# Performance work log

Hardware: AMD Instinct MI355X
Metric: run time of the kernel (lower is better)

## Reference

```python
import jax, jax.numpy as jnp
import numpy as np

B, N, DIM, H = 4, 2048, 1024, 8
HD = DIM // H
SCALE = HD ** -0.5


def setup_inputs() -> dict:
    key = jax.random.key(0)
    ks = jax.random.split(key, 9)
    inp = {
        "q": jax.random.normal(ks[0], (B, N, DIM), dtype=jnp.float32),
        "k": jax.random.normal(ks[1], (B, N, DIM), dtype=jnp.float32),
        "v": jax.random.normal(ks[2], (B, N, DIM), dtype=jnp.float32),
        "trans_mat": jax.random.normal(ks[3], (B, N, N), dtype=jnp.float32),
        # torch Linear weights: [out_features, in_features]; qkv_bias=False
        "Wq": jax.random.normal(ks[4], (DIM, DIM), dtype=jnp.float32) * (DIM ** -0.5),
        "Wk": jax.random.normal(ks[5], (DIM, DIM), dtype=jnp.float32) * (DIM ** -0.5),
        "Wv": jax.random.normal(ks[6], (DIM, DIM), dtype=jnp.float32) * (DIM ** -0.5),
        "Wp": jax.random.normal(ks[7], (DIM, DIM), dtype=jnp.float32) * (DIM ** -0.5),
        "bp": jax.random.normal(ks[8], (DIM,), dtype=jnp.float32) * 0.01,
    }
    return inp


def reference(q, k, v, trans_mat, Wq, Wk, Wv, Wp, bp):
    Bq, Nq, C = q.shape
    # project and split heads: [B, H, N, HD]
    qh = (q @ Wq.T).reshape(Bq, Nq, H, HD).transpose(0, 2, 1, 3)
    kh = (k @ Wk.T).reshape(Bq, -1, H, HD).transpose(0, 2, 1, 3)
    vh = (v @ Wv.T).reshape(Bq, -1, H, HD).transpose(0, 2, 1, 3)
    # scaled scores gated elementwise by trans_mat (broadcast over heads)
    scores = jnp.einsum("bhqd,bhkd->bhqk", qh, kh) * SCALE
    gated = scores * trans_mat[:, None, :, :]
    # softmax over full row, then zero out positions where gated == 0
    sm = jax.nn.softmax(gated, axis=-1)
    attn = jnp.where(gated != 0, sm, jnp.zeros((), dtype=sm.dtype))
    x = jnp.einsum("bhqk,bhkd->bhqd", attn, vh)
    x = x.transpose(0, 2, 1, 3).reshape(Bq, Nq, C)
    return x @ Wp.T + bp
```

## Files before the change

### kernel.cpp

```cpp
#include <hip/hip_runtime.h>
#include <hip/hip_bf16.h>
#include <stdint.h>

#define B_    4
#define N_    2048
#define DIM_  1024
#define H_    8
#define HD_   128
#define MTOK  (B_ * N_)
#define SCALE_  0.08838834764831845f
#define LOG2E_  1.4426950408889634f
#define QSCALE_ (SCALE_ * LOG2E_)

typedef unsigned short u16;
typedef __attribute__((ext_vector_type(4))) float f32x4;
typedef __attribute__((ext_vector_type(8))) short s16x8;
typedef __attribute__((ext_vector_type(8))) u16  u16x8;
typedef __attribute__((ext_vector_type(4))) u16  u16x4;

__device__ __forceinline__ u16 f2bf(float f) {
    uint32_t i = __builtin_bit_cast(uint32_t, f);
    return (u16)((i + 0x7FFFu + ((i >> 16) & 1u)) >> 16);
}

__device__ __forceinline__ void gl_lds16(const u16* g, u16* l) {
    __builtin_amdgcn_global_load_lds((const __attribute__((address_space(1))) void*)g,
                                     (__attribute__((address_space(3))) void*)l,
                                     16, 0, 0);
}

__global__ __launch_bounds__(256) void cvt_f32_bf16(const float* __restrict__ src,
                                                    u16* __restrict__ dst, int n) {
    int i = (blockIdx.x * 256 + threadIdx.x) * 4;
    int stride = gridDim.x * 256 * 4;
    for (; i < n; i += stride) {
        float4 v = *(const float4*)(src + i);
        u16x4 o;
        o.x = f2bf(v.x); o.y = f2bf(v.y); o.z = f2bf(v.z); o.w = f2bf(v.w);
        *(u16x4*)(dst + i) = o;
    }
}

template <int MODE>
__global__ __launch_bounds__(256) void gemm_bt(const u16* __restrict__ A,
                                               const u16* __restrict__ Bt,
                                               void* __restrict__ Cout,
                                               const float* __restrict__ bias,
                                               float scale, int M, int NN, int K) {
    __shared__ __align__(16) u16 lga[128 * 64];
    __shared__ __align__(16) u16 lgb[128 * 64];
    const int tid  = threadIdx.x;
    const int lane = tid & 63, wave = tid >> 6;
    const int wm = wave >> 1, wn = wave & 1;
    const int row0 = blockIdx.y * 128, col0 = blockIdx.x * 128;

    f32x4 acc[4][4] = {};

    auto stageLds = [&](const u16* G, u16* L, int rowbase, int k0) {
        #pragma unroll
        for (int i = 0; i < 4; i++) {
            int rb = wave * 32 + i * 8;
            int r  = rb + (lane >> 3);
            int cc = (lane & 7) ^ (lane >> 3);
            gl_lds16(G + (size_t)(rowbase + r) * K + k0 + cc * 8, L + rb * 64);
        }
    };

    for (int k0 = 0; k0 < K; k0 += 64) {
        stageLds(A,  lga, row0, k0);
        stageLds(Bt, lgb, col0, k0);
        __syncthreads();
        #pragma unroll
        for (int kk = 0; kk < 2; kk++) {
            s16x8 af[4], bfr[4];
            #pragma unroll
            for (int mi = 0; mi < 4; mi++) {
                int r = wm * 64 + mi * 16 + (lane & 15);
                int sc = (kk * 4 + (lane >> 4)) ^ (lane & 7);
                af[mi] = *(const s16x8*)(&lga[r * 64 + sc * 8]);
            }
            #pragma unroll
            for (int ni = 0; ni < 4; ni++) {
                int r = wn * 64 + ni * 16 + (lane & 15);
                int sc = (kk * 4 + (lane >> 4)) ^ (lane & 7);
                bfr[ni] = *(const s16x8*)(&lgb[r * 64 + sc * 8]);
            }
            #pragma unroll
            for (int mi = 0; mi < 4; mi++)
                #pragma unroll
                for (int ni = 0; ni < 4; ni++)
                    acc[mi][ni] = __builtin_amdgcn_mfma_f32_16x16x32_bf16(
                        af[mi], bfr[ni], acc[mi][ni], 0, 0, 0);
        }
        __syncthreads();
    }

    #pragma unroll
    for (int mi = 0; mi < 4; mi++) {
        #pragma unroll
        for (int ni = 0; ni < 4; ni++) {
            #pragma unroll
            for (int r = 0; r < 4; r++) {
                int grow = row0 + wm * 64 + mi * 16 + ((lane >> 4) << 2) + r;
                int gcol = col0 + wn * 64 + ni * 16 + (lane & 15);
                float vv = acc[mi][ni][r];
                if (MODE == 2) {
                    ((float*)Cout)[(size_t)grow * NN + gcol] = vv + bias[gcol];
                } else {
                    vv *= scale;
                    int bb = grow >> 11, n = grow & (N_ - 1);
                    int hh = gcol >> 7,  d = gcol & (HD_ - 1);
                    size_t idx = (MODE == 0)
                        ? ((size_t)(bb * H_ + hh) * N_ + n) * HD_ + d
                        : ((size_t)(bb * H_ + hh) * HD_ + d) * N_ + n;
                    ((u16*)Cout)[idx] = f2bf(vv);
                }
            }
        }
    }
}

__global__ __launch_bounds__(512) void attn_kernel(const u16* __restrict__ Qh,
                                                   const u16* __restrict__ Kh,
                                                   const u16* __restrict__ Vt,
                                                   const float* __restrict__ trans,
                                                   u16* __restrict__ xout) {
    __shared__ __align__(16) u16 kt[64 * 128];
    __shared__ __align__(16) u16 vt[128 * 64];
    __shared__ __align__(16) u16 plds[8][16 * 72];

    const int tid = threadIdx.x, lane = tid & 63, wave = tid >> 6;
    const int qt = blockIdx.x, h = blockIdx.y, b = blockIdx.z;
    const int qrow_base = qt * 128 + wave * 16;

    const u16* Qbh = Qh + (size_t)(b * H_ + h) * N_ * HD_;
    const u16* Kbh = Kh + (size_t)(b * H_ + h) * N_ * HD_;
    const u16* Vbh = Vt + (size_t)(b * H_ + h) * HD_ * N_;
    const float* trow = trans + (size_t)b * N_ * N_
                      + (size_t)(qrow_base + ((lane >> 4) << 2)) * N_ + (lane & 15);

    s16x8 qf[4];
    {
        int r = qrow_base + (lane & 15);
        #pragma unroll
        for (int kd = 0; kd < 4; kd++)
            qf[kd] = *(const s16x8*)(Qbh + (size_t)r * HD_ + kd * 32 + ((lane >> 4) << 3));
    }

    auto stageKV = [&](int kv0) {
        int rbk = wave * 8, rbv = wave * 16;
        #pragma unroll
        for (int j = 0; j < 2; j++) {
            int c = j * 64 + lane;
            int rk = rbk + (c >> 4);
            int ck = (c & 15) ^ (rk & 15);
            gl_lds16(Kbh + (size_t)(kv0 + rk) * HD_ + ck * 8, kt + rbk * 128 + j * 512);
            int rv = rbv + (c >> 3);
            int cv = (c & 7) ^ (rv & 7);
            gl_lds16(Vbh + (size_t)rv * N_ + kv0 + cv * 8, vt + rbv * 64 + j * 512);
        }
    };

    float m[4], l[4];
    #pragma unroll
    for (int r = 0; r < 4; r++) { m[r] = -3.0e38f; l[r] = 0.f; }
    f32x4 ao[8] = {};

    for (int kv0 = 0; kv0 < N_; kv0 += 64) {
        stageKV(kv0);
        __syncthreads();

        f32x4 s[4] = {};
        #pragma unroll
        for (int kd = 0; kd < 4; kd++)
            #pragma unroll
            for (int ni = 0; ni < 4; ni++) {
                int r = ni * 16 + (lane & 15);
                int sc = (kd * 4 + (lane >> 4)) ^ (lane & 15);
                s16x8 bfr = *(const s16x8*)(&kt[r * 128 + sc * 8]);
                s[ni] = __builtin_amdgcn_mfma_f32_16x16x32_bf16(qf[kd], bfr, s[ni], 0, 0, 0);
            }

        float pmax[4] = {-3.0e38f, -3.0e38f, -3.0e38f, -3.0e38f};
        #pragma unroll
        for (int ni = 0; ni < 4; ni++)
            #pragma unroll
            for (int r = 0; r < 4; r++) {
                float tt = trow[(size_t)r * N_ + kv0 + ni * 16];
                float gg = s[ni][r] * tt;
                s[ni][r] = gg;
                pmax[r] = fmaxf(pmax[r], gg);
            }
        #pragma unroll
        for (int r = 0; r < 4; r++) {
            float p = pmax[r];
            p = fmaxf(p, __shfl_xor(p, 1));
            p = fmaxf(p, __shfl_xor(p, 2));
            p = fmaxf(p, __shfl_xor(p, 4));
            p = fmaxf(p, __shfl_xor(p, 8));
            pmax[r] = p;
        }
        bool need = false;
        #pragma unroll
        for (int r = 0; r < 4; r++) need = need || (pmax[r] > m[r] + 8.0f);
        if (__any(need)) {
            #pragma unroll
            for (int r = 0; r < 4; r++) {
                float mn = fmaxf(m[r], pmax[r]);
                float sfv = __builtin_amdgcn_exp2f(m[r] - mn);
                m[r] = mn;
                l[r] *= sfv;
                #pragma unroll
                for (int t = 0; t < 8; t++) ao[t][r] *= sfv;
            }
        }
        float rowsum[4] = {0.f, 0.f, 0.f, 0.f};
        u16* pw = &plds[wave][0];
        #pragma unroll
        for (int ni = 0; ni < 4; ni++)
            #pragma unroll
            for (int r = 0; r < 4; r++) {
                float gg = s[ni][r];
                float e = __builtin_amdgcn_exp2f(gg - m[r]);
                rowsum[r] += e;
                float pe = (gg != 0.0f) ? e : 0.0f;
                pw[(((lane >> 4) << 2) + r) * 72 + ni * 16 + (lane & 15)] = f2bf(pe);
            }
        #pragma unroll
        for (int r = 0; r < 4; r++) {
            float ssum = rowsum[r];
            ssum += __shfl_xor(ssum, 1);
            ssum += __shfl_xor(ssum, 2);
            ssum += __shfl_xor(ssum, 4);
            ssum += __shfl_xor(ssum, 8);
            l[r] += ssum;
        }
        #pragma unroll
        for (int kk = 0; kk < 2; kk++) {
            s16x8 pa = *(const s16x8*)(&pw[(lane & 15) * 72 + kk * 32 + ((lane >> 4) << 3)]);
            #pragma unroll
            for (int t = 0; t < 8; t++) {
                int r = t * 16 + (lane & 15);
                int sc = (kk * 4 + (lane >> 4)) ^ (lane & 7);
                s16x8 vb = *(const s16x8*)(&vt[r * 64 + sc * 8]);
                ao[t] = __builtin_amdgcn_mfma_f32_16x16x32_bf16(pa, vb, ao[t], 0, 0, 0);
            }
        }
        __syncthreads();
    }

    #pragma unroll
    for (int r = 0; r < 4; r++) {
        float inv = 1.0f / l[r];
        int n = qrow_base + ((lane >> 4) << 2) + r;
        u16* orow = xout + ((size_t)(b * N_ + n)) * DIM_ + h * HD_;
        #pragma unroll
        for (int t = 0; t < 8; t++)
            orow[t * 16 + (lane & 15)] = f2bf(ao[t][r] * inv);
    }
}

extern "C" void kernel_launch(void* const* d_in, const int* in_sizes, int n_in,
                              void* d_out, int out_size, void* d_ws, size_t ws_size,
                              hipStream_t stream) {
    const float* q     = (const float*)d_in[0];
    const float* k     = (const float*)d_in[1];
    const float* v     = (const float*)d_in[2];
    const float* trans = (const float*)d_in[3];
    const float* Wq    = (const float*)d_in[4];
    const float* Wk    = (const float*)d_in[5];
    const float* Wv    = (const float*)d_in[6];
    const float* Wp    = (const float*)d_in[7];
    const float* bp    = (const float*)d_in[8];

    char* ws = (char*)d_ws;
    u16* tmp = (u16*)(ws);
    u16* wqb = (u16*)(ws + (16u << 20));
    u16* wkb = (u16*)(ws + (18u << 20));
    u16* wvb = (u16*)(ws + (20u << 20));
    u16* wpb = (u16*)(ws + (22u << 20));
    u16* QhB = (u16*)(ws + (24u << 20));
    u16* KhB = (u16*)(ws + (40u << 20));
    u16* VtB = (u16*)(ws + (56u << 20));
    u16* xb  = tmp;

    dim3 blk(256);
    cvt_f32_bf16<<<dim3(1024), blk, 0, stream>>>(Wq, wqb, DIM_ * DIM_);
    cvt_f32_bf16<<<dim3(1024), blk, 0, stream>>>(Wk, wkb, DIM_ * DIM_);
    cvt_f32_bf16<<<dim3(1024), blk, 0, stream>>>(Wv, wvb, DIM_ * DIM_);
    cvt_f32_bf16<<<dim3(1024), blk, 0, stream>>>(Wp, wpb, DIM_ * DIM_);

    dim3 pg(DIM_ / 128, MTOK / 128);

    cvt_f32_bf16<<<dim3(8192), blk, 0, stream>>>(q, tmp, MTOK * DIM_);
    gemm_bt<0><<<pg, blk, 0, stream>>>(tmp, wqb, QhB, nullptr, QSCALE_, MTOK, DIM_, DIM_);
    cvt_f32_bf16<<<dim3(8192), blk, 0, stream>>>(k, tmp, MTOK * DIM_);
    gemm_bt<0><<<pg, blk, 0, stream>>>(tmp, wkb, KhB, nullptr, 1.0f, MTOK, DIM_, DIM_);
    cvt_f32_bf16<<<dim3(8192), blk, 0, stream>>>(v, tmp, MTOK * DIM_);
    gemm_bt<1><<<pg, blk, 0, stream>>>(tmp, wvb, VtB, nullptr, 1.0f, MTOK, DIM_, DIM_);

    attn_kernel<<<dim3(N_ / 128, H_, B_), dim3(512), 0, stream>>>(QhB, KhB, VtB, trans, xb);

    gemm_bt<2><<<pg, blk, 0, stream>>>(xb, wpb, d_out, bp, 1.0f, MTOK, DIM_, DIM_);
}
```

Measured before the change: 289.8 us.

## Restructure attention to transposed 32x32 MFMA with register-resident P via permlane swap

Rewrites the attention kernel to compute S^T with 32x32x16 bf16 MFMAs so each lane owns one query row. Softmax max and sum then need only a single cross-half shuffle. The P matrix is packed to bf16 in registers and rearranged with v_permlane32_swap instead of a round trip through LDS. Each block now runs 4 waves of 32 rows instead of 8 waves of 16, the trans_mat tile is read with vectorized f32x4 loads, and the output is stored as u16x4. This raises accumulator register pressure and halves the waves per block.

Result: slower. 357.0 us (+23.2%).

```diff
diff --git a/kernel.cpp b/kernel.cpp
--- a/kernel.cpp
+++ b/kernel.cpp
@@ -13,14 +13,25 @@
 #define QSCALE_ (SCALE_ * LOG2E_)
 
 typedef unsigned short u16;
-typedef __attribute__((ext_vector_type(4))) float f32x4;
-typedef __attribute__((ext_vector_type(8))) short s16x8;
-typedef __attribute__((ext_vector_type(8))) u16  u16x8;
-typedef __attribute__((ext_vector_type(4))) u16  u16x4;
+typedef __attribute__((ext_vector_type(4)))  float f32x4;
+typedef __attribute__((ext_vector_type(16))) float f32x16;
+typedef __attribute__((ext_vector_type(8)))  short s16x8;
+typedef __attribute__((ext_vector_type(8)))  u16  u16x8;
+typedef __attribute__((ext_vector_type(4)))  u16  u16x4;
+typedef __attribute__((ext_vector_type(4)))  unsigned u32x4;
 
 __device__ __forceinline__ u16 f2bf(float f) {
     uint32_t i = __builtin_bit_cast(uint32_t, f);
     return (u16)((i + 0x7FFFu + ((i >> 16) & 1u)) >> 16);
+}
+
+__device__ __forceinline__ unsigned pk_bf16(float a, float b) {
+    unsigned r;
+    asm("v_cvt_pk_bf16_f32 %0, %1, %2" : "=v"(r) : "v"(a), "v"(b));
+    return r;
+}
+__device__ __forceinline__ void pl32_swap(unsigned &a, unsigned &b) {
+    asm volatile("v_permlane32_swap_b32 %0, %1" : "+v"(a), "+v"(b));
 }
 
 __device__ __forceinline__ void gl_lds16(const u16* g, u16* l) {
@@ -120,144 +131,144 @@
     }
 }
 
-__global__ __launch_bounds__(512) void attn_kernel(const u16* __restrict__ Qh,
+__global__ __launch_bounds__(256) void attn_kernel(const u16* __restrict__ Qh,
                                                    const u16* __restrict__ Kh,
                                                    const u16* __restrict__ Vt,
                                                    const float* __restrict__ trans,
                                                    u16* __restrict__ xout) {
     __shared__ __align__(16) u16 kt[64 * 128];
     __shared__ __align__(16) u16 vt[128 * 64];
-    __shared__ __align__(16) u16 plds[8][16 * 72];
 
     const int tid = threadIdx.x, lane = tid & 63, wave = tid >> 6;
-    const int qt = blockIdx.x, h = blockIdx.y, b = blockIdx.z;
-    const int qrow_base = qt * 128 + wave * 16;
-
-    const u16* Qbh = Qh + (size_t)(b * H_ + h) * N_ * HD_;
-    const u16* Kbh = Kh + (size_t)(b * H_ + h) * N_ * HD_;
-    const u16* Vbh = Vt + (size_t)(b * H_ + h) * HD_ * N_;
-    const float* trow = trans + (size_t)b * N_ * N_
-                      + (size_t)(qrow_base + ((lane >> 4) << 2)) * N_ + (lane & 15);
-
-    s16x8 qf[4];
-    {
-        int r = qrow_base + (lane & 15);
-        #pragma unroll
-        for (int kd = 0; kd < 4; kd++)
-            qf[kd] = *(const s16x8*)(Qbh + (size_t)r * HD_ + kd * 32 + ((lane >> 4) << 3));
-    }
+    const int lq = lane & 31, hl = lane >> 5;
+    const int qt = blockIdx.x, hh = blockIdx.y, b = blockIdx.z;
+    const int q = qt * 128 + wave * 32 + lq;
+
+    const u16* Qbh = Qh + (size_t)(b * H_ + hh) * N_ * HD_;
+    const u16* Kbh = Kh + (size_t)(b * H_ + hh) * N_ * HD_;
+    const u16* Vbh = Vt + (size_t)(b * H_ + hh) * HD_ * N_;
+    const float* trow = trans + (size_t)b * N_ * N_ + (size_t)q * N_;
+
+    s16x8 qf[8];
+    #pragma unroll
+    for (int s = 0; s < 8; s++)
+        qf[s] = *(const s16x8*)(Qbh + (size_t)q * HD_ + s * 16 + hl * 8);
 
     auto stageKV = [&](int kv0) {
-        int rbk = wave * 8, rbv = wave * 16;
-        #pragma unroll
-        for (int j = 0; j < 2; j++) {
-            int c = j * 64 + lane;
-            int rk = rbk + (c >> 4);
-            int ck = (c & 15) ^ (rk & 15);
-            gl_lds16(Kbh + (size_t)(kv0 + rk) * HD_ + ck * 8, kt + rbk * 128 + j * 512);
-            int rv = rbv + (c >> 3);
-            int cv = (c & 7) ^ (rv & 7);
-            gl_lds16(Vbh + (size_t)rv * N_ + kv0 + cv * 8, vt + rbv * 64 + j * 512);
+        #pragma unroll
+        for (int i = 0; i < 4; i++) {
+            int rk = wave * 16 + i * 4 + (lane >> 4);
+            int ck = (lane & 15) ^ (rk & 15);
+            gl_lds16(Kbh + (size_t)(kv0 + rk) * HD_ + ck * 8,
+                     kt + (wave * 16 + i * 4) * 128);
+            int rv = wave * 32 + i * 8 + (lane >> 3);
+            int cv = (lane & 7) ^ (rv & 7);
+            gl_lds16(Vbh + (size_t)rv * N_ + kv0 + cv * 8,
+                     vt + (wave * 32 + i * 8) * 64);
         }
     };
 
-    float m[4], l[4];
-    #pragma unroll
-    for (int r = 0; r < 4; r++) { m[r] = -3.0e38f; l[r] = 0.f; }
-    f32x4 ao[8] = {};
+    float m = -3.0e38f, l = 0.f;
+    f32x16 aoT[4] = {};
 
     for (int kv0 = 0; kv0 < N_; kv0 += 64) {
+        f32x4 tt[2][4];
+        #pragma unroll
+        for (int ni = 0; ni < 2; ni++)
+            #pragma unroll
+            for (int r2 = 0; r2 < 4; r2++)
+                tt[ni][r2] = *(const f32x4*)(trow + kv0 + ni * 32 + r2 * 8 + hl * 4);
+
         stageKV(kv0);
         __syncthreads();
 
-        f32x4 s[4] = {};
-        #pragma unroll
-        for (int kd = 0; kd < 4; kd++)
-            #pragma unroll
-            for (int ni = 0; ni < 4; ni++) {
-                int r = ni * 16 + (lane & 15);
-                int sc = (kd * 4 + (lane >> 4)) ^ (lane & 15);
-                s16x8 bfr = *(const s16x8*)(&kt[r * 128 + sc * 8]);
-                s[ni] = __builtin_amdgcn_mfma_f32_16x16x32_bf16(qf[kd], bfr, s[ni], 0, 0, 0);
-            }
-
-        float pmax[4] = {-3.0e38f, -3.0e38f, -3.0e38f, -3.0e38f};
-        #pragma unroll
-        for (int ni = 0; ni < 4; ni++)
-            #pragma unroll
-            for (int r = 0; r < 4; r++) {
-                float tt = trow[(size_t)r * N_ + kv0 + ni * 16];
-                float gg = s[ni][r] * tt;
-                s[ni][r] = gg;
-                pmax[r] = fmaxf(pmax[r], gg);
-            }
-        #pragma unroll
-        for (int r = 0; r < 4; r++) {
-            float p = pmax[r];
-            p = fmaxf(p, __shfl_xor(p, 1));
-            p = fmaxf(p, __shfl_xor(p, 2));
-            p = fmaxf(p, __shfl_xor(p, 4));
-            p = fmaxf(p, __shfl_xor(p, 8));
-            pmax[r] = p;
-        }
-        bool need = false;
-        #pragma unroll
-        for (int r = 0; r < 4; r++) need = need || (pmax[r] > m[r] + 8.0f);
-        if (__any(need)) {
-            #pragma unroll
-            for (int r = 0; r < 4; r++) {
-                float mn = fmaxf(m[r], pmax[r]);
-                float sfv = __builtin_amdgcn_exp2f(m[r] - mn);
-                m[r] = mn;
-                l[r] *= sfv;
+        f32x16 sT[2] = {};
+        #pragma unroll
+        for (int s = 0; s < 8; s++)
+            #pragma unroll
+            for (int ni = 0; ni < 2; ni++) {
+                int r = ni * 32 + lq;
+                int slot = (2 * s + hl) ^ (r & 15);
+                s16x8 kf = *(const s16x8*)(&kt[r * 128 + slot * 8]);
+                sT[ni] = __builtin_amdgcn_mfma_f32_32x32x16_bf16(kf, qf[s], sT[ni], 0, 0, 0);
+            }
+
+        float mx = -3.0e38f;
+        #pragma unroll
+        for (int ni = 0; ni < 2; ni++)
+            #pragma unroll
+            for (int r2 = 0; r2 < 4; r2++)
                 #pragma unroll
-                for (int t = 0; t < 8; t++) ao[t][r] *= sfv;
-            }
-        }
-        float rowsum[4] = {0.f, 0.f, 0.f, 0.f};
-        u16* pw = &plds[wave][0];
-        #pragma unroll
-        for (int ni = 0; ni < 4; ni++)
-            #pragma unroll
-            for (int r = 0; r < 4; r++) {
-                float gg = s[ni][r];
-                float e = __builtin_amdgcn_exp2f(gg - m[r]);
-                rowsum[r] += e;
-                float pe = (gg != 0.0f) ? e : 0.0f;
-                pw[(((lane >> 4) << 2) + r) * 72 + ni * 16 + (lane & 15)] = f2bf(pe);
-            }
-        #pragma unroll
-        for (int r = 0; r < 4; r++) {
-            float ssum = rowsum[r];
-            ssum += __shfl_xor(ssum, 1);
-            ssum += __shfl_xor(ssum, 2);
-            ssum += __shfl_xor(ssum, 4);
-            ssum += __shfl_xor(ssum, 8);
-            l[r] += ssum;
-        }
-        #pragma unroll
-        for (int kk = 0; kk < 2; kk++) {
-            s16x8 pa = *(const s16x8*)(&pw[(lane & 15) * 72 + kk * 32 + ((lane >> 4) << 3)]);
-            #pragma unroll
-            for (int t = 0; t < 8; t++) {
-                int r = t * 16 + (lane & 15);
-                int sc = (kk * 4 + (lane >> 4)) ^ (lane & 7);
-                s16x8 vb = *(const s16x8*)(&vt[r * 64 + sc * 8]);
-                ao[t] = __builtin_amdgcn_mfma_f32_16x16x32_bf16(pa, vb, ao[t], 0, 0, 0);
-            }
-        }
+                for (int e = 0; e < 4; e++) {
+                    float g = sT[ni][r2 * 4 + e] * tt[ni][r2][e];
+                    sT[ni][r2 * 4 + e] = g;
+                    mx = fmaxf(mx, g);
+                }
+        mx = fmaxf(mx, __shfl_xor(mx, 32));
+
+        if (__any(mx > m + 8.0f)) {
+            float mn = fmaxf(m, mx);
+            float sfv = __builtin_amdgcn_exp2f(m - mn);
+            m = mn;
+            l *= sfv;
+            #pragma unroll
+            for (int dt = 0; dt < 4; dt++)
+                #pragma unroll
+                for (int e = 0; e < 16; e++) aoT[dt][e] *= sfv;
+        }
+
+        float rs = 0.f;
+        #pragma unroll
+        for (int ni = 0; ni < 2; ni++)
+            #pragma unroll
+            for (int e = 0; e < 16; e++) {
+                float g = sT[ni][e];
+                float p = __builtin_amdgcn_exp2f(g - m);
+                rs += p;
+                sT[ni][e] = (g != 0.0f) ? p : 0.0f;
+            }
+        rs += __shfl_xor(rs, 32);
+        l += rs;
+
+        s16x8 pfrag[4];
+        #pragma unroll
+        for (int sp = 0; sp < 4; sp++) {
+            const int ni = sp >> 1;
+            const int ru = (2 * sp) & 3, rv = (2 * sp + 1) & 3;
+            unsigned u0 = pk_bf16(sT[ni][ru * 4 + 0], sT[ni][ru * 4 + 1]);
+            unsigned u1 = pk_bf16(sT[ni][ru * 4 + 2], sT[ni][ru * 4 + 3]);
+            unsigned v0 = pk_bf16(sT[ni][rv * 4 + 0], sT[ni][rv * 4 + 1]);
+            unsigned v1 = pk_bf16(sT[ni][rv * 4 + 2], sT[ni][rv * 4 + 3]);
+            pl32_swap(u0, v0);
+            pl32_swap(u1, v1);
+            u32x4 w = {u0, u1, v0, v1};
+            pfrag[sp] = __builtin_bit_cast(s16x8, w);
+        }
+
+        #pragma unroll
+        for (int dt = 0; dt < 4; dt++)
+            #pragma unroll
+            for (int sp = 0; sp < 4; sp++) {
+                int r = dt * 32 + lq;
+                int slot = (2 * sp + hl) ^ (r & 7);
+                s16x8 vf = *(const s16x8*)(&vt[r * 64 + slot * 8]);
+                aoT[dt] = __builtin_amdgcn_mfma_f32_32x32x16_bf16(vf, pfrag[sp], aoT[dt], 0, 0, 0);
+            }
         __syncthreads();
     }
 
+    float inv = 1.0f / l;
+    u16* orow = xout + ((size_t)(b * N_ + q)) * DIM_ + hh * HD_;
     #pragma unroll
-    for (int r = 0; r < 4; r++) {
-        float inv = 1.0f / l[r];
-        int n = qrow_base + ((lane >> 4) << 2) + r;
-        u16* orow = xout + ((size_t)(b * N_ + n)) * DIM_ + h * HD_;
-        #pragma unroll
-        for (int t = 0; t < 8; t++)
-            orow[t * 16 + (lane & 15)] = f2bf(ao[t][r] * inv);
-    }
+    for (int dt = 0; dt < 4; dt++)
+        #pragma unroll
+        for (int r2 = 0; r2 < 4; r2++) {
+            u16x4 ov;
+            #pragma unroll
+            for (int e = 0; e < 4; e++)
+                ov[e] = f2bf(aoT[dt][r2 * 4 + e] * inv);
+            *(u16x4*)(orow + dt * 32 + r2 * 8 + hl * 4) = ov;
+        }
 }
 
 extern "C" void kernel_launch(void* const* d_in, const int* in_sizes, int n_in,
@@ -299,7 +310,7 @@
     cvt_f32_bf16<<<dim3(8192), blk, 0, stream>>>(v, tmp, MTOK * DIM_);
     gemm_bt<1><<<pg, blk, 0, stream>>>(tmp, wvb, VtB, nullptr, 1.0f, MTOK, DIM_, DIM_);
 
-    attn_kernel<<<dim3(N_ / 128, H_, B_), dim3(512), 0, stream>>>(QhB, KhB, VtB, trans, xb);
+    attn_kernel<<<dim3(N_ / 128, H_, B_), dim3(256), 0, stream>>>(QhB, KhB, VtB, trans, xb);
 
     gemm_bt<2><<<pg, blk, 0, stream>>>(xb, wpb, d_out, bp, 1.0f, MTOK, DIM_, DIM_);
 }
```

## Rewrite attention with swapped 32x32 MFMA, double-buffered KV, and transposed gate matrix

Applied to the files above, without the earlier changes.

Replaces the attention kernel with one that computes S^T = K·Q^T using 32x32x16 bf16 MFMAs, so each lane owns a single query row. That removes per-row cross-lane reductions, and permlane32 swaps build the P operand in registers instead of going through LDS. K/V tiles are double-buffered in LDS and blocks are remapped for locality. The gate matrix is pre-transposed by a new kernel so that per-lane gate loads coalesce. Weight conversion is merged into one launch. The new path needs a larger workspace, otherwise it falls back to the old kernel, and the transpose adds a full extra pass over trans_mat.

Result: faster. 276.2 us (-4.7%).

```diff
diff --git a/kernel.cpp b/kernel.cpp
--- a/kernel.cpp
+++ b/kernel.cpp
@@ -13,16 +13,25 @@
 #define QSCALE_ (SCALE_ * LOG2E_)
 
 typedef unsigned short u16;
-typedef __attribute__((ext_vector_type(4))) float f32x4;
-typedef __attribute__((ext_vector_type(8))) short s16x8;
-typedef __attribute__((ext_vector_type(8))) u16  u16x8;
-typedef __attribute__((ext_vector_type(4))) u16  u16x4;
+typedef __attribute__((ext_vector_type(4)))  float f32x4;
+typedef __attribute__((ext_vector_type(16))) float f32x16;
+typedef __attribute__((ext_vector_type(8)))  short s16x8;
+typedef __attribute__((ext_vector_type(8)))  u16  u16x8;
+typedef __attribute__((ext_vector_type(4)))  u16  u16x4;
+typedef __attribute__((ext_vector_type(4)))  unsigned u32x4;
 
 __device__ __forceinline__ u16 f2bf(float f) {
     uint32_t i = __builtin_bit_cast(uint32_t, f);
     return (u16)((i + 0x7FFFu + ((i >> 16) & 1u)) >> 16);
 }
-
+__device__ __forceinline__ unsigned pk_bf16(float a, float b) {
+    unsigned r;
+    asm("v_cvt_pk_bf16_f32 %0, %1, %2" : "=v"(r) : "v"(a), "v"(b));
+    return r;
+}
+__device__ __forceinline__ void pl32_swap(unsigned &a, unsigned &b) {
+    asm volatile("v_permlane32_swap_b32 %0, %1" : "+v"(a), "+v"(b));
+}
 __device__ __forceinline__ void gl_lds16(const u16* g, u16* l) {
     __builtin_amdgcn_global_load_lds((const __attribute__((address_space(1))) void*)g,
                                      (__attribute__((address_space(3))) void*)l,
@@ -39,6 +48,36 @@
         o.x = f2bf(v.x); o.y = f2bf(v.y); o.z = f2bf(v.z); o.w = f2bf(v.w);
         *(u16x4*)(dst + i) = o;
     }
+}
+
+__global__ __launch_bounds__(256) void cvt_w4(const float* __restrict__ s0,
+                                              const float* __restrict__ s1,
+                                              const float* __restrict__ s2,
+                                              const float* __restrict__ s3,
+                                              u16* __restrict__ dst) {
+    const float* s = blockIdx.y == 0 ? s0 : blockIdx.y == 1 ? s1 : blockIdx.y == 2 ? s2 : s3;
+    u16* d = dst + (size_t)blockIdx.y * (DIM_ * DIM_);
+    int i = (blockIdx.x * 256 + threadIdx.x) * 8;
+    float4 a = *(const float4*)(s + i);
+    float4 b = *(const float4*)(s + i + 4);
+    u32x4 w = {pk_bf16(a.x, a.y), pk_bf16(a.z, a.w), pk_bf16(b.x, b.y), pk_bf16(b.z, b.w)};
+    *(u16x8*)(d + i) = __builtin_bit_cast(u16x8, w);
+}
+
+__global__ __launch_bounds__(256) void transpose_f32(const float* __restrict__ in,
+                                                     float* __restrict__ out) {
+    __shared__ float t[64][65];
+    const int r0 = blockIdx.y * 64, c0 = blockIdx.x * 64;
+    const float* ib = in + (size_t)blockIdx.z * N_ * N_;
+    float* ob = out + (size_t)blockIdx.z * N_ * N_;
+    const int lr = threadIdx.x >> 6, lc = threadIdx.x & 63;
+    #pragma unroll
+    for (int i = 0; i < 16; i++)
+        t[i * 4 + lr][lc] = ib[(size_t)(r0 + i * 4 + lr) * N_ + c0 + lc];
+    __syncthreads();
+    #pragma unroll
+    for (int i = 0; i < 16; i++)
+        ob[(size_t)(c0 + i * 4 + lr) * N_ + r0 + lc] = t[lc][i * 4 + lr];
 }
 
 template <int MODE>
@@ -120,11 +159,165 @@
     }
 }
 
-__global__ __launch_bounds__(512) void attn_kernel(const u16* __restrict__ Qh,
-                                                   const u16* __restrict__ Kh,
-                                                   const u16* __restrict__ Vt,
-                                                   const float* __restrict__ trans,
-                                                   u16* __restrict__ xout) {
+__global__ __launch_bounds__(256, 2) void attn_swapped(const u16* __restrict__ Qh,
+                                                       const u16* __restrict__ Kh,
+                                                       const u16* __restrict__ Vt,
+                                                       const float* __restrict__ transT,
+                                                       u16* __restrict__ xout) {
+    __shared__ __align__(16) u16 kt[2][64 * 128];
+    __shared__ __align__(16) u16 vt[2][128 * 64];
+
+    const int tid = threadIdx.x, lane = tid & 63, wave = tid >> 6;
+    const int lq = lane & 31, hl = lane >> 5;
+
+    int lin = blockIdx.x + 16 * (blockIdx.y + 8 * blockIdx.z);
+    int nl  = (lin & 7) * 64 + (lin >> 3);
+    const int qt = nl & 15, hh = (nl >> 4) & 7, b = nl >> 7;
+    const int q0 = qt * 128 + wave * 32;
+    const int q  = q0 + lq;
+
+    const u16* Qbh = Qh + (size_t)(b * H_ + hh) * N_ * HD_;
+    const u16* Kbh = Kh + (size_t)(b * H_ + hh) * N_ * HD_;
+    const u16* Vbh = Vt + (size_t)(b * H_ + hh) * HD_ * N_;
+    const float* tTq = transT + (size_t)b * N_ * N_ + q;
+
+    s16x8 qf[8];
+    #pragma unroll
+    for (int s = 0; s < 8; s++)
+        qf[s] = *(const s16x8*)(Qbh + (size_t)q * HD_ + s * 16 + hl * 8);
+
+    auto stageKV = [&](int kv0, int bi) {
+        #pragma unroll
+        for (int i = 0; i < 4; i++) {
+            int rk = wave * 16 + i * 4 + (lane >> 4);
+            int ck = (lane & 15) ^ (rk & 15) ^ ((rk & 16) >> 2);
+            gl_lds16(Kbh + (size_t)(kv0 + rk) * HD_ + ck * 8,
+                     &kt[bi][(wave * 16 + i * 4) * 128]);
+            int rv = wave * 32 + i * 8 + (lane >> 3);
+            int cv = (lane & 7) ^ (rv & 7) ^ ((rv >> 3) & 3);
+            gl_lds16(Vbh + (size_t)rv * N_ + kv0 + cv * 8,
+                     &vt[bi][(wave * 32 + i * 8) * 64]);
+        }
+    };
+
+    const int mKl = (lq & 15) ^ ((lq & 16) >> 2);
+    const int mVl = (lq & 7) ^ ((lq >> 3) & 3);
+
+    float m = -3.0e38f, l = 0.f;
+    f32x16 aoT[4] = {};
+
+    stageKV(0, 0);
+    __syncthreads();
+
+    for (int it = 0; it < N_ / 64; it++) {
+        const int kv0 = it * 64, cur = it & 1;
+        if (it + 1 < N_ / 64) stageKV(kv0 + 64, cur ^ 1);
+
+        float tt[2][16];
+        #pragma unroll
+        for (int ni = 0; ni < 2; ni++)
+            #pragma unroll
+            for (int idx = 0; idx < 16; idx++) {
+                int kv = (idx & 3) + 8 * (idx >> 2) + 4 * hl + 32 * ni;
+                tt[ni][idx] = tTq[(size_t)(kv0 + kv) * N_];
+            }
+
+        f32x16 sT[2] = {};
+        __builtin_amdgcn_s_setprio(1);
+        #pragma unroll
+        for (int s = 0; s < 8; s++)
+            #pragma unroll
+            for (int ni = 0; ni < 2; ni++) {
+                int r = ni * 32 + lq;
+                int slot = (2 * s + hl) ^ mKl;
+                s16x8 kf = *(const s16x8*)(&kt[cur][r * 128 + slot * 8]);
+                sT[ni] = __builtin_amdgcn_mfma_f32_32x32x16_bf16(kf, qf[s], sT[ni], 0, 0, 0);
+            }
+        __builtin_amdgcn_s_setprio(0);
+
+        float mx = -3.0e38f;
+        #pragma unroll
+        for (int ni = 0; ni < 2; ni++)
+            #pragma unroll
+            for (int idx = 0; idx < 16; idx++) {
+                float g = sT[ni][idx] * tt[ni][idx];
+                sT[ni][idx] = g;
+                mx = fmaxf(mx, g);
+            }
+        mx = fmaxf(mx, __shfl_xor(mx, 32));
+
+        if (__any(mx > m + 8.0f)) {
+            float mn = fmaxf(m, mx);
+            float sfv = __builtin_amdgcn_exp2f(m - mn);
+            m = mn;
+            l *= sfv;
+            #pragma unroll
+            for (int dt = 0; dt < 4; dt++)
+                #pragma unroll
+                for (int e = 0; e < 16; e++) aoT[dt][e] *= sfv;
+        }
+
+        float rs = 0.f;
+        #pragma unroll
+        for (int ni = 0; ni < 2; ni++)
+            #pragma unroll
+            for (int e = 0; e < 16; e++) {
+                float g = sT[ni][e];
+                float p = __builtin_amdgcn_exp2f(g - m);
+                rs += p;
+                sT[ni][e] = (g != 0.0f) ? p : 0.0f;
+            }
+        rs += __shfl_xor(rs, 32);
+        l += rs;
+
+        s16x8 pfrag[4];
+        #pragma unroll
+        for (int sp = 0; sp < 4; sp++) {
+            const int ni = sp >> 1;
+            const int ru = (2 * sp) & 3, rv2 = (2 * sp + 1) & 3;
+            unsigned u0 = pk_bf16(sT[ni][ru * 4 + 0], sT[ni][ru * 4 + 1]);
+            unsigned u1 = pk_bf16(sT[ni][ru * 4 + 2], sT[ni][ru * 4 + 3]);
+            unsigned v0 = pk_bf16(sT[ni][rv2 * 4 + 0], sT[ni][rv2 * 4 + 1]);
+            unsigned v1 = pk_bf16(sT[ni][rv2 * 4 + 2], sT[ni][rv2 * 4 + 3]);
+            pl32_swap(u0, v0);
+            pl32_swap(u1, v1);
+            u32x4 w = {u0, u1, v0, v1};
+            pfrag[sp] = __builtin_bit_cast(s16x8, w);
+        }
+
+        __builtin_amdgcn_s_setprio(1);
+        #pragma unroll
+        for (int dt = 0; dt < 4; dt++)
+            #pragma unroll
+            for (int sp = 0; sp < 4; sp++) {
+                int r = dt * 32 + lq;
+                int slot = (2 * sp + hl) ^ mVl;
+                s16x8 vf = *(const s16x8*)(&vt[cur][r * 64 + slot * 8]);
+                aoT[dt] = __builtin_amdgcn_mfma_f32_32x32x16_bf16(vf, pfrag[sp], aoT[dt], 0, 0, 0);
+            }
+        __builtin_amdgcn_s_setprio(0);
+        __syncthreads();
+    }
+
+    float inv = 1.0f / l;
+    u16* orow = xout + ((size_t)(b * N_ + q)) * DIM_ + hh * HD_;
+    #pragma unroll
+    for (int dt = 0; dt < 4; dt++)
+        #pragma unroll
+        for (int r2 = 0; r2 < 4; r2++) {
+            u16x4 ov;
+            #pragma unroll
+            for (int e = 0; e < 4; e++)
+                ov[e] = f2bf(aoT[dt][r2 * 4 + e] * inv);
+            *(u16x4*)(orow + dt * 32 + r2 * 8 + hl * 4) = ov;
+        }
+}
+
+__global__ __launch_bounds__(512) void attn_fb(const u16* __restrict__ Qh,
+                                               const u16* __restrict__ Kh,
+                                               const u16* __restrict__ Vt,
+                                               const float* __restrict__ trans,
+                                               u16* __restrict__ xout) {
     __shared__ __align__(16) u16 kt[64 * 128];
     __shared__ __align__(16) u16 vt[128 * 64];
     __shared__ __align__(16) u16 plds[8][16 * 72];
@@ -146,17 +339,14 @@
         for (int kd = 0; kd < 4; kd++)
             qf[kd] = *(const s16x8*)(Qbh + (size_t)r * HD_ + kd * 32 + ((lane >> 4) << 3));
     }
-
     auto stageKV = [&](int kv0) {
         int rbk = wave * 8, rbv = wave * 16;
         #pragma unroll
         for (int j = 0; j < 2; j++) {
             int c = j * 64 + lane;
-            int rk = rbk + (c >> 4);
-            int ck = (c & 15) ^ (rk & 15);
+            int rk = rbk + (c >> 4), ck = (c & 15) ^ (rk & 15);
             gl_lds16(Kbh + (size_t)(kv0 + rk) * HD_ + ck * 8, kt + rbk * 128 + j * 512);
-            int rv = rbv + (c >> 3);
-            int cv = (c & 7) ^ (rv & 7);
+            int rv = rbv + (c >> 3), cv = (c & 7) ^ (rv & 7);
             gl_lds16(Vbh + (size_t)rv * N_ + kv0 + cv * 8, vt + rbv * 64 + j * 512);
         }
     };
@@ -169,7 +359,6 @@
     for (int kv0 = 0; kv0 < N_; kv0 += 64) {
         stageKV(kv0);
         __syncthreads();
-
         f32x4 s[4] = {};
         #pragma unroll
         for (int kd = 0; kd < 4; kd++)
@@ -180,7 +369,6 @@
                 s16x8 bfr = *(const s16x8*)(&kt[r * 128 + sc * 8]);
                 s[ni] = __builtin_amdgcn_mfma_f32_16x16x32_bf16(qf[kd], bfr, s[ni], 0, 0, 0);
             }
-
         float pmax[4] = {-3.0e38f, -3.0e38f, -3.0e38f, -3.0e38f};
         #pragma unroll
         for (int ni = 0; ni < 4; ni++)
@@ -208,8 +396,7 @@
             for (int r = 0; r < 4; r++) {
                 float mn = fmaxf(m[r], pmax[r]);
                 float sfv = __builtin_amdgcn_exp2f(m[r] - mn);
-                m[r] = mn;
-                l[r] *= sfv;
+                m[r] = mn; l[r] *= sfv;
                 #pragma unroll
                 for (int t = 0; t < 8; t++) ao[t][r] *= sfv;
             }
@@ -241,14 +428,13 @@
             #pragma unroll
             for (int t = 0; t < 8; t++) {
                 int r = t * 16 + (lane & 15);
-                int sc = (kk * 4 + (lane >> 4)) ^ (lane & 7);
+                int sc = (kk * 4 + (lane >> 4)) ^ (r & 7);
                 s16x8 vb = *(const s16x8*)(&vt[r * 64 + sc * 8]);
                 ao[t] = __builtin_amdgcn_mfma_f32_16x16x32_bf16(pa, vb, ao[t], 0, 0, 0);
             }
         }
         __syncthreads();
     }
-
     #pragma unroll
     for (int r = 0; r < 4; r++) {
         float inv = 1.0f / l[r];
@@ -282,13 +468,12 @@
     u16* QhB = (u16*)(ws + (24u << 20));
     u16* KhB = (u16*)(ws + (40u << 20));
     u16* VtB = (u16*)(ws + (56u << 20));
+    float* tT = (float*)(ws + (72u << 20));
     u16* xb  = tmp;
+    const bool big = ws_size >= (136ull << 20);
 
     dim3 blk(256);
-    cvt_f32_bf16<<<dim3(1024), blk, 0, stream>>>(Wq, wqb, DIM_ * DIM_);
-    cvt_f32_bf16<<<dim3(1024), blk, 0, stream>>>(Wk, wkb, DIM_ * DIM_);
-    cvt_f32_bf16<<<dim3(1024), blk, 0, stream>>>(Wv, wvb, DIM_ * DIM_);
-    cvt_f32_bf16<<<dim3(1024), blk, 0, stream>>>(Wp, wpb, DIM_ * DIM_);
+    cvt_w4<<<dim3(512, 4), blk, 0, stream>>>(Wq, Wk, Wv, Wp, wqb);
 
     dim3 pg(DIM_ / 128, MTOK / 128);
 
@@ -299,7 +484,12 @@
     cvt_f32_bf16<<<dim3(8192), blk, 0, stream>>>(v, tmp, MTOK * DIM_);
     gemm_bt<1><<<pg, blk, 0, stream>>>(tmp, wvb, VtB, nullptr, 1.0f, MTOK, DIM_, DIM_);
 
-    attn_kernel<<<dim3(N_ / 128, H_, B_), dim3(512), 0, stream>>>(QhB, KhB, VtB, trans, xb);
+    if (big) {
+        transpose_f32<<<dim3(N_ / 64, N_ / 64, B_), blk, 0, stream>>>(trans, tT);
+        attn_swapped<<<dim3(16, 8, 4), dim3(256), 0, stream>>>(QhB, KhB, VtB, tT, xb);
+    } else {
+        attn_fb<<<dim3(N_ / 128, H_, B_), dim3(512), 0, stream>>>(QhB, KhB, VtB, trans, xb);
+    }
 
     gemm_bt<2><<<pg, blk, 0, stream>>>(xb, wpb, d_out, bp, 1.0f, MTOK, DIM_, DIM_);
 }
```
